# Kernel optimization log

Measured on AMD Instinct MI355X. Metric: run time of the kernel, lower is better.

## Reference

```python
import jax, jax.numpy as jnp
import numpy as np

BIGNET_DIM = 1024
N_LAYERS = 18   # 6 blocks * 3 QLoRALinear
N_LN = 5
GROUPS = 64     # 1024 / group_size(16)
GS = 16
RANK = 32
BATCH = 16384
EPS = 1e-5


def dequant(qw, scale):
    # qw: [O, G, gs] int 0..15, scale: [O, G] per-group max-abs norm
    w = (qw.astype(jnp.float32) / 15.0 * 2.0 - 1.0) * scale[..., None]
    return w.reshape(qw.shape[0], -1)  # [O, I]


def qlora_linear(x, qw, scale, b, a_w, b_w):
    w = dequant(qw, scale)                      # [O, I]
    base = x @ w.T + b                          # [N, O]
    lora = (x @ a_w.T) @ b_w.T                  # [N, r] @ [r, O]
    return base + lora


def layernorm(h, g, b):
    mu = h.mean(-1, keepdims=True)
    var = jnp.mean((h - mu) ** 2, -1, keepdims=True)
    return (h - mu) * jax.lax.rsqrt(var + EPS) * g + b


def setup_inputs() -> dict:
    key = jax.random.key(0)
    ks = jax.random.split(key, 8)
    x = jax.random.normal(ks[0], (BATCH, BIGNET_DIM), jnp.float32)
    qw = jax.random.randint(ks[1], (N_LAYERS, BIGNET_DIM, GROUPS, GS), 0, 16, jnp.int32)
    scale = jax.random.uniform(ks[2], (N_LAYERS, BIGNET_DIM, GROUPS), jnp.float32) * 0.05
    bias = jax.random.normal(ks[3], (N_LAYERS, BIGNET_DIM), jnp.float32) * 0.02
    la = jax.random.normal(ks[4], (N_LAYERS, RANK, BIGNET_DIM), jnp.float32) * (2.0 / BIGNET_DIM) ** 0.5
    # note: torch zero-inits lora_b; use small random values so the LoRA path is testable
    lb = jax.random.normal(ks[5], (N_LAYERS, BIGNET_DIM, RANK), jnp.float32) * 0.01
    ln_w = jnp.ones((N_LN, BIGNET_DIM), jnp.float32)
    ln_b = jnp.zeros((N_LN, BIGNET_DIM), jnp.float32)
    return {"x": x, "scale": scale, "bias": bias, "la": la, "lb": lb,
            "ln_w": ln_w, "ln_b": ln_b, "qw": qw}


def reference(x, scale, bias, la, lb, ln_w, ln_b, qw):
    h = x
    li = 0
    for blk in range(6):
        r = h
        for j in range(3):
            h = qlora_linear(h, qw[li], scale[li], bias[li], la[li], lb[li])
            li += 1
            if j < 2:
                h = jax.nn.relu(h)
        h = h + r
        if blk < 5:
            h = layernorm(h, ln_w[blk], ln_b[blk])
    return h
```

## Files before the change

### kernel.cpp

```cpp
#include <hip/hip_runtime.h>

typedef unsigned short UST;
typedef __attribute__((ext_vector_type(8))) __bf16 bf16x8;
typedef __attribute__((ext_vector_type(4))) float f32x4;

__device__ __forceinline__ float bf2f(UST u) {
    union { unsigned int i; float f; } v; v.i = ((unsigned int)u) << 16; return v.f;
}
__device__ __forceinline__ UST f2bf(float f) {
    union { float f; unsigned int i; } v; v.f = f;
    return (UST)((v.i + 0x7fffu + ((v.i >> 16) & 1u)) >> 16);
}

__device__ __forceinline__ void gl2lds16(const UST* g, UST* l) {
    __builtin_amdgcn_global_load_lds(
        (const __attribute__((address_space(1))) unsigned int*)g,
        (__attribute__((address_space(3))) unsigned int*)l, 16, 0, 0);
}

#define WB4 asm volatile("s_waitcnt vmcnt(4)\n\ts_barrier" ::: "memory")
#define WB0 asm volatile("s_waitcnt vmcnt(0)\n\ts_barrier" ::: "memory")
#define LGB asm volatile("s_waitcnt lgkmcnt(0)\n\ts_barrier" ::: "memory")

__global__ __launch_bounds__(256) void prep_w(
    const int* __restrict__ qw, const float* __restrict__ scale,
    const float* __restrict__ la, const float* __restrict__ lb,
    UST* __restrict__ wp)
{
    int l = blockIdx.x, ot = blockIdx.y, it = blockIdx.z;
    __shared__ float cs[64 * 128];
    __shared__ float sc_s[128 * 8];
    int t = threadIdx.x;
    int wave = t >> 6, lane = t & 63;
    int wm = wave >> 1, wn = wave & 1;
    int la15 = lane & 15, qa = lane >> 4;

    {
        int e = t * 4;
        int o = e >> 3, g = e & 7;
        const float* sb = scale + ((size_t)l * 1024 + ot * 128 + o) * 64 + it * 8 + g;
        *(float4*)&sc_s[e] = *(const float4*)sb;
    }

    bf16x8 af[4];
    const float* lbL = lb + ((size_t)l * 1024 + ot * 128 + wm * 64 + la15) * 32 + qa * 8;
    #pragma unroll
    for (int mi = 0; mi < 4; mi++) {
        float4 u0 = *(const float4*)(lbL + mi * 16 * 32);
        float4 u1 = *(const float4*)(lbL + mi * 16 * 32 + 4);
        union { bf16x8 v; UST u[8]; } A;
        A.u[0] = f2bf(u0.x); A.u[1] = f2bf(u0.y); A.u[2] = f2bf(u0.z); A.u[3] = f2bf(u0.w);
        A.u[4] = f2bf(u1.x); A.u[5] = f2bf(u1.y); A.u[6] = f2bf(u1.z); A.u[7] = f2bf(u1.w);
        af[mi] = A.v;
    }

    bf16x8 bfr[4];
    const float* laL = la + ((size_t)l * 32 + qa * 8) * 1024 + it * 128 + wn * 64 + la15;
    #pragma unroll
    for (int ni = 0; ni < 4; ni++) {
        union { bf16x8 v; UST u[8]; } B;
        #pragma unroll
        for (int j = 0; j < 8; j++) B.u[j] = f2bf(laL[(size_t)j * 1024 + ni * 16]);
        bfr[ni] = B.v;
    }

    f32x4 acc[4][4];
    #pragma unroll
    for (int mi = 0; mi < 4; mi++)
        #pragma unroll
        for (int ni = 0; ni < 4; ni++) {
            acc[mi][ni] = (f32x4){0.f, 0.f, 0.f, 0.f};
            acc[mi][ni] = __builtin_amdgcn_mfma_f32_16x16x32_bf16(
                af[mi], bfr[ni], acc[mi][ni], 0, 0, 0);
        }

    int qv[4][4][4];
    const int* qL = qw + (size_t)l * 1048576;
    int obase = ot * 128 + wm * 64, ibase = it * 128 + wn * 64;
    #pragma unroll
    for (int mi = 0; mi < 4; mi++)
        #pragma unroll
        for (int ni = 0; ni < 4; ni++)
            #pragma unroll
            for (int r2 = 0; r2 < 4; r2++)
                qv[mi][ni][r2] = qL[(size_t)(obase + mi * 16 + qa * 4 + r2) * 1024
                                    + ibase + ni * 16 + la15];

    __syncthreads();

    int cc = t & 15, rw = t >> 4;
    UST* wL = wp + (size_t)l * 1048576;
    #pragma unroll
    for (int h = 0; h < 2; ++h) {
        if (wm == h) {
            #pragma unroll
            for (int mi = 0; mi < 4; mi++)
                #pragma unroll
                for (int ni = 0; ni < 4; ni++) {
                    int colx = (wn * 64 + ni * 16 + la15) ^ (qa << 4);
                    #pragma unroll
                    for (int r2 = 0; r2 < 4; r2++) {
                        int rl = mi * 16 + qa * 4 + r2;
                        float s = sc_s[(h * 64 + rl) * 8 + wn * 4 + ni];
                        float w = ((float)qv[mi][ni][r2] * (2.0f / 15.0f) - 1.0f) * s
                                  + acc[mi][ni][r2];
                        cs[rl * 128 + colx] = w;
                    }
                }
        }
        LGB;
        #pragma unroll
        for (int g = 0; g < 4; ++g) {
            int rl = g * 16 + rw;
            int swz = ((rl >> 2) & 3) << 2;
            int gr0 = ((cc * 2) ^ swz) * 4;
            float4 v0 = *(const float4*)&cs[rl * 128 + gr0];
            float4 v1 = *(const float4*)&cs[rl * 128 + gr0 + 4];
            uint4 pk;
            pk.x = (unsigned)f2bf(v0.x) | ((unsigned)f2bf(v0.y) << 16);
            pk.y = (unsigned)f2bf(v0.z) | ((unsigned)f2bf(v0.w) << 16);
            pk.z = (unsigned)f2bf(v1.x) | ((unsigned)f2bf(v1.y) << 16);
            pk.w = (unsigned)f2bf(v1.z) | ((unsigned)f2bf(v1.w) << 16);
            *(uint4*)&wL[(size_t)(ot * 128 + h * 64 + rl) * 1024 + it * 128 + cc * 8] = pk;
        }
        LGB;
    }
}

__global__ __launch_bounds__(256) void f32_to_bf16(const float* __restrict__ x,
                                                   UST* __restrict__ o)
{
    size_t i = ((size_t)blockIdx.x * 256 + threadIdx.x) * 4;
    float4 v = *(const float4*)(x + i);
    *(ushort4*)(o + i) = make_ushort4(f2bf(v.x), f2bf(v.y), f2bf(v.z), f2bf(v.w));
}

#define BK 32

__global__ __launch_bounds__(512, 2) void gemm_ep(
    const UST* __restrict__ X, const UST* __restrict__ W,
    const float* __restrict__ bias,
    UST* __restrict__ outb, const UST* __restrict__ resid,
    float* __restrict__ outf, int mode)
{
    const int K = 1024;
    __shared__ UST smem[32768];
    int tid = threadIdx.x;
    int wave = tid >> 6, lane = tid & 63;
    int wm = wave >> 1, wn = wave & 1;
    int la15 = lane & 15, qa = lane >> 4;

    int bid = blockIdx.x;
    int xcd = bid & 7, idx = bid >> 3;
    int bm = xcd * 8 + (idx & 7);
    int bn = idx >> 3;

    int c0 = tid, c1 = tid + 512;
    int r0 = c0 >> 2, k0c = ((c0 & 3) ^ ((r0 >> 1) & 3)) * 8;
    int r1 = c1 >> 2, k1c = ((c1 & 3) ^ ((r1 >> 1) & 3)) * 8;
    const UST* gA0 = X + (size_t)(bm * 256 + r0) * K + k0c;
    const UST* gA1 = X + (size_t)(bm * 256 + r1) * K + k1c;
    const UST* gB0 = W + (size_t)(bn * 256 + r0) * K + k0c;
    const UST* gB1 = W + (size_t)(bn * 256 + r1) * K + k1c;

    int offA[4], offB[8];
    #pragma unroll
    for (int i = 0; i < 4; i++) {
        int ra = wm * 64 + i * 16 + la15;
        offA[i] = ra * 32 + ((qa ^ ((ra >> 1) & 3)) * 8);
    }
    #pragma unroll
    for (int i = 0; i < 8; i++) {
        int rb = wn * 128 + i * 16 + la15;
        offB[i] = rb * 32 + ((qa ^ ((rb >> 1) & 3)) * 8);
    }

    f32x4 acc[4][8];
    #pragma unroll
    for (int i = 0; i < 4; i++)
        #pragma unroll
        for (int j = 0; j < 8; j++) acc[i][j] = (f32x4){0.f, 0.f, 0.f, 0.f};

    auto issue = [&](int kk, int buf) {
        UST* dA = smem + buf * 16384;
        UST* dB = dA + 8192;
        gl2lds16(gA0 + kk, dA + c0 * 8);
        gl2lds16(gA1 + kk, dA + c1 * 8);
        gl2lds16(gB0 + kk, dB + c0 * 8);
        gl2lds16(gB1 + kk, dB + c1 * 8);
    };
    auto compute = [&](int buf) {
        const UST* pA = smem + buf * 16384;
        const UST* pB = pA + 8192;
        bf16x8 af[4], bfr[8];
        #pragma unroll
        for (int mi = 0; mi < 4; mi++) af[mi] = *(const bf16x8*)&pA[offA[mi]];
        #pragma unroll
        for (int ni = 0; ni < 8; ni++) bfr[ni] = *(const bf16x8*)&pB[offB[ni]];
        #pragma unroll
        for (int mi = 0; mi < 4; mi++)
            #pragma unroll
            for (int ni = 0; ni < 8; ni++)
                acc[mi][ni] = __builtin_amdgcn_mfma_f32_16x16x32_bf16(
                    af[mi], bfr[ni], acc[mi][ni], 0, 0, 0);
    };

    issue(0, 0);
    #pragma unroll 2
    for (int it = 0; it < 31; ++it) {
        int cur = it & 1;
        issue((it + 1) * BK, cur ^ 1);
        WB4;
        compute(cur);
        LGB;
    }
    WB0;
    compute(1);
    LGB;

    float* cs = (float*)smem;
    int cc = tid & 31, rw = tid >> 5;
    int gcolb = bn * 256 + cc * 8;
    float4 bv0 = *(const float4*)&bias[gcolb];
    float4 bv1 = *(const float4*)&bias[gcolb + 4];

    #pragma unroll
    for (int h = 0; h < 4; ++h) {
        if (wm == h) {
            #pragma unroll
            for (int mi = 0; mi < 4; mi++)
                #pragma unroll
                for (int ni = 0; ni < 8; ni++) {
                    int colx = (wn * 128 + ni * 16 + la15) ^ (qa << 4);
                    #pragma unroll
                    for (int r2 = 0; r2 < 4; r2++) {
                        int rl = mi * 16 + qa * 4 + r2;
                        cs[rl * 256 + colx] = acc[mi][ni][r2];
                    }
                }
        }
        LGB;
        #pragma unroll
        for (int g = 0; g < 4; ++g) {
            int rl = g * 16 + rw;
            int swz = ((rl >> 2) & 3) << 2;
            int gr0 = ((cc * 2) ^ swz) * 4;
            float4 v0 = *(const float4*)&cs[rl * 256 + gr0];
            float4 v1 = *(const float4*)&cs[rl * 256 + gr0 + 4];
            float o0 = v0.x + bv0.x, o1 = v0.y + bv0.y;
            float o2 = v0.z + bv0.z, o3 = v0.w + bv0.w;
            float o4 = v1.x + bv1.x, o5 = v1.y + bv1.y;
            float o6 = v1.z + bv1.z, o7 = v1.w + bv1.w;
            if (mode == 0) {
                o0 = fmaxf(o0, 0.f); o1 = fmaxf(o1, 0.f);
                o2 = fmaxf(o2, 0.f); o3 = fmaxf(o3, 0.f);
                o4 = fmaxf(o4, 0.f); o5 = fmaxf(o5, 0.f);
                o6 = fmaxf(o6, 0.f); o7 = fmaxf(o7, 0.f);
            }
            int grow = bm * 256 + h * 64 + rl;
            size_t base = (size_t)grow * 1024 + gcolb;
            if (mode == 2) {
                ushort4 rv0 = *(const ushort4*)&resid[base];
                ushort4 rv1 = *(const ushort4*)&resid[base + 4];
                o0 += bf2f(rv0.x); o1 += bf2f(rv0.y);
                o2 += bf2f(rv0.z); o3 += bf2f(rv0.w);
                o4 += bf2f(rv1.x); o5 += bf2f(rv1.y);
                o6 += bf2f(rv1.z); o7 += bf2f(rv1.w);
                *(float4*)&outf[base] = make_float4(o0, o1, o2, o3);
                *(float4*)&outf[base + 4] = make_float4(o4, o5, o6, o7);
            } else {
                uint4 pk;
                pk.x = (unsigned)f2bf(o0) | ((unsigned)f2bf(o1) << 16);
                pk.y = (unsigned)f2bf(o2) | ((unsigned)f2bf(o3) << 16);
                pk.z = (unsigned)f2bf(o4) | ((unsigned)f2bf(o5) << 16);
                pk.w = (unsigned)f2bf(o6) | ((unsigned)f2bf(o7) << 16);
                *(uint4*)&outb[base] = pk;
            }
        }
        LGB;
    }
}

__global__ __launch_bounds__(256) void ln_res(
    const UST* __restrict__ h3, UST* __restrict__ r,
    const float* __restrict__ g, const float* __restrict__ b)
{
    int row = blockIdx.x;
    int t = threadIdx.x;
    int lane = t & 63, wave = t >> 6;
    const ushort4* hp = (const ushort4*)(h3 + (size_t)row * 1024);
    ushort4* rp = (ushort4*)(r + (size_t)row * 1024);
    ushort4 hv = hp[t], rv = rp[t];
    float u0 = bf2f(hv.x) + bf2f(rv.x);
    float u1 = bf2f(hv.y) + bf2f(rv.y);
    float u2 = bf2f(hv.z) + bf2f(rv.z);
    float u3 = bf2f(hv.w) + bf2f(rv.w);

    float s = u0 + u1 + u2 + u3;
    #pragma unroll
    for (int off = 32; off > 0; off >>= 1) s += __shfl_down(s, off, 64);
    __shared__ float red[8];
    if (lane == 0) red[wave] = s;
    __syncthreads();
    float mean = (red[0] + red[1] + red[2] + red[3]) * (1.0f / 1024.0f);

    float d0 = u0 - mean, d1 = u1 - mean, d2 = u2 - mean, d3 = u3 - mean;
    float vs = d0 * d0 + d1 * d1 + d2 * d2 + d3 * d3;
    #pragma unroll
    for (int off = 32; off > 0; off >>= 1) vs += __shfl_down(vs, off, 64);
    if (lane == 0) red[4 + wave] = vs;
    __syncthreads();
    float var = (red[4] + red[5] + red[6] + red[7]) * (1.0f / 1024.0f);
    float rstd = rsqrtf(var + 1e-5f);

    int i0 = t * 4;
    ushort4 o;
    o.x = f2bf(d0 * rstd * g[i0 + 0] + b[i0 + 0]);
    o.y = f2bf(d1 * rstd * g[i0 + 1] + b[i0 + 1]);
    o.z = f2bf(d2 * rstd * g[i0 + 2] + b[i0 + 2]);
    o.w = f2bf(d3 * rstd * g[i0 + 3] + b[i0 + 3]);
    rp[t] = o;
}

extern "C" void kernel_launch(void* const* d_in, const int* in_sizes, int n_in,
                              void* d_out, int out_size, void* d_ws, size_t ws_size,
                              hipStream_t stream) {
    const float* x     = (const float*)d_in[0];
    const float* scale = (const float*)d_in[1];
    const float* bias  = (const float*)d_in[2];
    const float* la    = (const float*)d_in[3];
    const float* lb    = (const float*)d_in[4];
    const float* ln_w  = (const float*)d_in[5];
    const float* ln_b  = (const float*)d_in[6];
    const int*   qw    = (const int*)d_in[7];

    const int M = in_sizes[0] / 1024;
    const size_t WPB = (size_t)18 * 1024 * 1024 * 2;
    const size_t ACT = (size_t)M * 1024 * 2;

    UST* wp = (UST*)d_ws;
    UST* A  = (UST*)((char*)d_ws + WPB);
    UST* Cb = (UST*)((char*)d_ws + WPB + ACT);
    UST* Bb = (UST*)d_out;

    prep_w<<<dim3(18, 8, 8), 256, 0, stream>>>(qw, scale, la, lb, wp);
    f32_to_bf16<<<(M * 1024) / (256 * 4), 256, 0, stream>>>(x, A);

    int nblk = (M / 256) * 4;
    int li = 0;
    for (int blk = 0; blk < 6; ++blk) {
        gemm_ep<<<nblk, 512, 0, stream>>>(
            A, wp + (size_t)li * 1024 * 1024, bias + li * 1024, Bb, nullptr, nullptr, 0);
        li++;
        gemm_ep<<<nblk, 512, 0, stream>>>(
            Bb, wp + (size_t)li * 1024 * 1024, bias + li * 1024, Cb, nullptr, nullptr, 0);
        li++;
        if (blk < 5) {
            gemm_ep<<<nblk, 512, 0, stream>>>(
                Cb, wp + (size_t)li * 1024 * 1024, bias + li * 1024, Bb, nullptr, nullptr, 1);
            li++;
            ln_res<<<M, 256, 0, stream>>>(Bb, A, ln_w + blk * 1024, ln_b + blk * 1024);
        } else {
            gemm_ep<<<nblk, 512, 0, stream>>>(
                Cb, wp + (size_t)li * 1024 * 1024, bias + li * 1024, nullptr, A,
                (float*)d_out, 2);
            li++;
        }
    }
}
```

Measured before the change: 985.9 us.

## Fuse residual add into GEMM epilogue, wave-per-row LayerNorm, coalesce prep_w loads

The residual add moves from the LayerNorm kernel into the mode-1 GEMM epilogue, so the LN kernel no longer reads the residual buffer. LayerNorm is rewritten to use one wavefront per row, with a single-pass sum and sum-of-squares and no block barriers. The weight prep kernel now stages LoRA-A through shared memory and reads qw with coalesced vector loads, applying dequantization in the packing stage. The cost is a less numerically stable variance formula, and bf16 rounding of the residual sum before LN.

```diff
diff --git a/kernel.cpp b/kernel.cpp
--- a/kernel.cpp
+++ b/kernel.cpp
@@ -28,7 +28,7 @@
     UST* __restrict__ wp)
 {
     int l = blockIdx.x, ot = blockIdx.y, it = blockIdx.z;
-    __shared__ float cs[64 * 128];
+    __shared__ float buf[8192];
     __shared__ float sc_s[128 * 8];
     int t = threadIdx.x;
     int wave = t >> 6, lane = t & 63;
@@ -40,6 +40,21 @@
         int o = e >> 3, g = e & 7;
         const float* sb = scale + ((size_t)l * 1024 + ot * 128 + o) * 64 + it * 8 + g;
         *(float4*)&sc_s[e] = *(const float4*)sb;
+    }
+
+    float* last = buf;
+    {
+        const float* laB = la + (size_t)l * 32 * 1024 + it * 128;
+        #pragma unroll
+        for (int p = 0; p < 4; p++) {
+            int e = t * 4 + p * 1024;
+            int r = e >> 7, i0 = e & 127;
+            float4 v = *(const float4*)(laB + (size_t)r * 1024 + i0);
+            last[(i0 + 0) * 33 + r] = v.x;
+            last[(i0 + 1) * 33 + r] = v.y;
+            last[(i0 + 2) * 33 + r] = v.z;
+            last[(i0 + 3) * 33 + r] = v.w;
+        }
     }
 
     bf16x8 af[4];
@@ -54,13 +69,16 @@
         af[mi] = A.v;
     }
 
+    __syncthreads();
+
     bf16x8 bfr[4];
-    const float* laL = la + ((size_t)l * 32 + qa * 8) * 1024 + it * 128 + wn * 64 + la15;
     #pragma unroll
     for (int ni = 0; ni < 4; ni++) {
+        int iloc = wn * 64 + ni * 16 + la15;
+        const float* pp = &last[iloc * 33 + qa * 8];
         union { bf16x8 v; UST u[8]; } B;
         #pragma unroll
-        for (int j = 0; j < 8; j++) B.u[j] = f2bf(laL[(size_t)j * 1024 + ni * 16]);
+        for (int j = 0; j < 8; j++) B.u[j] = f2bf(pp[j]);
         bfr[ni] = B.v;
     }
 
@@ -74,24 +92,23 @@
                 af[mi], bfr[ni], acc[mi][ni], 0, 0, 0);
         }
 
-    int qv[4][4][4];
-    const int* qL = qw + (size_t)l * 1048576;
-    int obase = ot * 128 + wm * 64, ibase = it * 128 + wn * 64;
-    #pragma unroll
-    for (int mi = 0; mi < 4; mi++)
-        #pragma unroll
-        for (int ni = 0; ni < 4; ni++)
-            #pragma unroll
-            for (int r2 = 0; r2 < 4; r2++)
-                qv[mi][ni][r2] = qL[(size_t)(obase + mi * 16 + qa * 4 + r2) * 1024
-                                    + ibase + ni * 16 + la15];
-
     __syncthreads();
 
+    float* cs = buf;
     int cc = t & 15, rw = t >> 4;
     UST* wL = wp + (size_t)l * 1048576;
+    const int* qL = qw + (size_t)l * 1048576;
     #pragma unroll
     for (int h = 0; h < 2; ++h) {
+        int4 qd[4][2];
+        #pragma unroll
+        for (int g = 0; g < 4; g++) {
+            int rl = g * 16 + rw;
+            const int* qrow = qL + (size_t)(ot * 128 + h * 64 + rl) * 1024
+                              + it * 128 + cc * 8;
+            qd[g][0] = *(const int4*)qrow;
+            qd[g][1] = *(const int4*)(qrow + 4);
+        }
         if (wm == h) {
             #pragma unroll
             for (int mi = 0; mi < 4; mi++)
@@ -101,10 +118,7 @@
                     #pragma unroll
                     for (int r2 = 0; r2 < 4; r2++) {
                         int rl = mi * 16 + qa * 4 + r2;
-                        float s = sc_s[(h * 64 + rl) * 8 + wn * 4 + ni];
-                        float w = ((float)qv[mi][ni][r2] * (2.0f / 15.0f) - 1.0f) * s
-                                  + acc[mi][ni][r2];
-                        cs[rl * 128 + colx] = w;
+                        cs[rl * 128 + colx] = acc[mi][ni][r2];
                     }
                 }
         }
@@ -116,11 +130,21 @@
             int gr0 = ((cc * 2) ^ swz) * 4;
             float4 v0 = *(const float4*)&cs[rl * 128 + gr0];
             float4 v1 = *(const float4*)&cs[rl * 128 + gr0 + 4];
+            float s = sc_s[(h * 64 + rl) * 8 + (cc >> 1)];
+            float t2 = s * (2.0f / 15.0f);
+            float o0 = fmaf((float)qd[g][0].x, t2, v0.x - s);
+            float o1 = fmaf((float)qd[g][0].y, t2, v0.y - s);
+            float o2 = fmaf((float)qd[g][0].z, t2, v0.z - s);
+            float o3 = fmaf((float)qd[g][0].w, t2, v0.w - s);
+            float o4 = fmaf((float)qd[g][1].x, t2, v1.x - s);
+            float o5 = fmaf((float)qd[g][1].y, t2, v1.y - s);
+            float o6 = fmaf((float)qd[g][1].z, t2, v1.z - s);
+            float o7 = fmaf((float)qd[g][1].w, t2, v1.w - s);
             uint4 pk;
-            pk.x = (unsigned)f2bf(v0.x) | ((unsigned)f2bf(v0.y) << 16);
-            pk.y = (unsigned)f2bf(v0.z) | ((unsigned)f2bf(v0.w) << 16);
-            pk.z = (unsigned)f2bf(v1.x) | ((unsigned)f2bf(v1.y) << 16);
-            pk.w = (unsigned)f2bf(v1.z) | ((unsigned)f2bf(v1.w) << 16);
+            pk.x = (unsigned)f2bf(o0) | ((unsigned)f2bf(o1) << 16);
+            pk.y = (unsigned)f2bf(o2) | ((unsigned)f2bf(o3) << 16);
+            pk.z = (unsigned)f2bf(o4) | ((unsigned)f2bf(o5) << 16);
+            pk.w = (unsigned)f2bf(o6) | ((unsigned)f2bf(o7) << 16);
             *(uint4*)&wL[(size_t)(ot * 128 + h * 64 + rl) * 1024 + it * 128 + cc * 8] = pk;
         }
         LGB;
@@ -259,13 +283,15 @@
             }
             int grow = bm * 256 + h * 64 + rl;
             size_t base = (size_t)grow * 1024 + gcolb;
-            if (mode == 2) {
+            if (mode != 0) {
                 ushort4 rv0 = *(const ushort4*)&resid[base];
                 ushort4 rv1 = *(const ushort4*)&resid[base + 4];
                 o0 += bf2f(rv0.x); o1 += bf2f(rv0.y);
                 o2 += bf2f(rv0.z); o3 += bf2f(rv0.w);
                 o4 += bf2f(rv1.x); o5 += bf2f(rv1.y);
                 o6 += bf2f(rv1.z); o7 += bf2f(rv1.w);
+            }
+            if (mode == 2) {
                 *(float4*)&outf[base] = make_float4(o0, o1, o2, o3);
                 *(float4*)&outf[base + 4] = make_float4(o4, o5, o6, o7);
             } else {
@@ -281,45 +307,48 @@
     }
 }
 
-__global__ __launch_bounds__(256) void ln_res(
-    const UST* __restrict__ h3, UST* __restrict__ r,
+__global__ __launch_bounds__(256) void ln_only(
+    const UST* __restrict__ s, UST* __restrict__ r,
     const float* __restrict__ g, const float* __restrict__ b)
 {
-    int row = blockIdx.x;
-    int t = threadIdx.x;
-    int lane = t & 63, wave = t >> 6;
-    const ushort4* hp = (const ushort4*)(h3 + (size_t)row * 1024);
-    ushort4* rp = (ushort4*)(r + (size_t)row * 1024);
-    ushort4 hv = hp[t], rv = rp[t];
-    float u0 = bf2f(hv.x) + bf2f(rv.x);
-    float u1 = bf2f(hv.y) + bf2f(rv.y);
-    float u2 = bf2f(hv.z) + bf2f(rv.z);
-    float u3 = bf2f(hv.w) + bf2f(rv.w);
-
-    float s = u0 + u1 + u2 + u3;
-    #pragma unroll
-    for (int off = 32; off > 0; off >>= 1) s += __shfl_down(s, off, 64);
-    __shared__ float red[8];
-    if (lane == 0) red[wave] = s;
-    __syncthreads();
-    float mean = (red[0] + red[1] + red[2] + red[3]) * (1.0f / 1024.0f);
-
-    float d0 = u0 - mean, d1 = u1 - mean, d2 = u2 - mean, d3 = u3 - mean;
-    float vs = d0 * d0 + d1 * d1 + d2 * d2 + d3 * d3;
-    #pragma unroll
-    for (int off = 32; off > 0; off >>= 1) vs += __shfl_down(vs, off, 64);
-    if (lane == 0) red[4 + wave] = vs;
-    __syncthreads();
-    float var = (red[4] + red[5] + red[6] + red[7]) * (1.0f / 1024.0f);
+    int wave = threadIdx.x >> 6, lane = threadIdx.x & 63;
+    int row = blockIdx.x * 4 + wave;
+    const UST* sp = s + (size_t)row * 1024;
+    UST* rp = r + (size_t)row * 1024;
+
+    float v[16];
+    float sum = 0.f, ss = 0.f;
+    #pragma unroll
+    for (int k = 0; k < 4; k++) {
+        ushort4 hv = *(const ushort4*)(sp + k * 256 + lane * 4);
+        float a0 = bf2f(hv.x), a1 = bf2f(hv.y), a2 = bf2f(hv.z), a3 = bf2f(hv.w);
+        v[k * 4 + 0] = a0; v[k * 4 + 1] = a1; v[k * 4 + 2] = a2; v[k * 4 + 3] = a3;
+        sum += a0 + a1 + a2 + a3;
+        ss += a0 * a0 + a1 * a1 + a2 * a2 + a3 * a3;
+    }
+    #pragma unroll
+    for (int off = 32; off > 0; off >>= 1) {
+        sum += __shfl_down(sum, off, 64);
+        ss  += __shfl_down(ss, off, 64);
+    }
+    sum = __shfl(sum, 0, 64);
+    ss  = __shfl(ss, 0, 64);
+    float mean = sum * (1.0f / 1024.0f);
+    float var = ss * (1.0f / 1024.0f) - mean * mean;
     float rstd = rsqrtf(var + 1e-5f);
 
-    int i0 = t * 4;
-    ushort4 o;
-    o.x = f2bf(d0 * rstd * g[i0 + 0] + b[i0 + 0]);
-    o.y = f2bf(d1 * rstd * g[i0 + 1] + b[i0 + 1]);
-    o.z = f2bf(d2 * rstd * g[i0 + 2] + b[i0 + 2]);
-    o.w = f2bf(d3 * rstd * g[i0 + 3] + b[i0 + 3]);
-    rp[t] = o;
+    #pragma unroll
+    for (int k = 0; k < 4; k++) {
+        int c = k * 256 + lane * 4;
+        float4 gv = *(const float4*)(g + c);
+        float4 bv = *(const float4*)(b + c);
+        ushort4 o;
+        o.x = f2bf((v[k * 4 + 0] - mean) * rstd * gv.x + bv.x);
+        o.y = f2bf((v[k * 4 + 1] - mean) * rstd * gv.y + bv.y);
+        o.z = f2bf((v[k * 4 + 2] - mean) * rstd * gv.z + bv.z);
+        o.w = f2bf((v[k * 4 + 3] - mean) * rstd * gv.w + bv.w);
+        *(ushort4*)(rp + c) = o;
+    }
 }
 
 extern "C" void kernel_launch(void* const* d_in, const int* in_sizes, int n_in,
@@ -357,9 +386,9 @@
         li++;
         if (blk < 5) {
             gemm_ep<<<nblk, 512, 0, stream>>>(
-                Cb, wp + (size_t)li * 1024 * 1024, bias + li * 1024, Bb, nullptr, nullptr, 1);
+                Cb, wp + (size_t)li * 1024 * 1024, bias + li * 1024, Bb, A, nullptr, 1);
             li++;
-            ln_res<<<M, 256, 0, stream>>>(Bb, A, ln_w + blk * 1024, ln_b + blk * 1024);
+            ln_only<<<M / 4, 256, 0, stream>>>(Bb, A, ln_w + blk * 1024, ln_b + blk * 1024);
         } else {
             gemm_ep<<<nblk, 512, 0, stream>>>(
                 Cb, wp + (size_t)li * 1024 * 1024, bias + li * 1024, nullptr, A,
```

New measurement: 940.9 us. 1.05x faster.
